# Optimization experiments

Measured on AMD Instinct MI355X. Metric: run time of the kernel, lower is better.

## Reference

```python
import jax, jax.numpy as jnp
import numpy as np

B, S, D = 4, 2048, 1024


def setup_inputs() -> dict:
    key = jax.random.key(0)
    ks = jax.random.split(key, 7)
    scale = 1.0 / np.sqrt(D)  # mimic torch Linear default init scale
    x = jax.random.normal(ks[0], (B, S, D), dtype=jnp.float32)
    Wq = jax.random.uniform(ks[1], (D, D), jnp.float32, -scale, scale)
    bq = jax.random.uniform(ks[2], (D,), jnp.float32, -scale, scale)
    Wk = jax.random.uniform(ks[3], (D, D), jnp.float32, -scale, scale)
    bk = jax.random.uniform(ks[4], (D,), jnp.float32, -scale, scale)
    Wv = jax.random.uniform(ks[5], (D, D), jnp.float32, -scale, scale)
    bv = jax.random.uniform(ks[6], (D,), jnp.float32, -scale, scale)
    return {"x": x, "Wq": Wq, "bq": bq, "Wk": Wk, "bk": bk, "Wv": Wv, "bv": bv}


def reference(x, Wq, bq, Wk, bk, Wv, bv):
    # Linear projections (torch Linear: x @ W.T + b; here W stored as [in, out])
    q = jnp.einsum("bsd,de->bse", x, Wq) + bq
    k = jnp.einsum("bsd,de->bse", x, Wk) + bk
    v = jnp.einsum("bsd,de->bse", x, Wv) + bv
    # NOTE: original module applies NO 1/sqrt(d) scaling — faithful to source.
    scores = jnp.einsum("bqd,bkd->bqk", q, k)  # [B, S, S]
    attn = jax.nn.softmax(scores, axis=-1)
    return jnp.einsum("bqk,bkd->bqd", attn, v)
```

## Files before the change

### kernel.cpp

```cpp
#include <hip/hip_runtime.h>
#include <stdint.h>

typedef unsigned short ushort_t;
typedef _Float16 f16;
typedef __attribute__((ext_vector_type(8))) _Float16 half8;
typedef __attribute__((ext_vector_type(4))) _Float16 half4;
typedef __attribute__((ext_vector_type(4))) float float4v;

#define AS1 __attribute__((address_space(1)))
#define AS3 __attribute__((address_space(3)))

static __device__ __forceinline__ void gload16(const void* g, void* l) {
    __builtin_amdgcn_global_load_lds((const AS1 unsigned int*)g,
                                     (AS3 unsigned int*)l, 16, 0, 0);
}

static __device__ __forceinline__ void barrier_nodrain() {
    __builtin_amdgcn_sched_barrier(0);
    __builtin_amdgcn_s_barrier();
    __builtin_amdgcn_sched_barrier(0);
}

template<int IM, int OUT, bool BIAS>
__global__ __launch_bounds__(256, IM == 8 ? 2 : 3)
void gemm_k(const f16* __restrict__ A, const f16* __restrict__ B,
            const float* __restrict__ bias,
            float* __restrict__ Cf, f16* __restrict__ Ch, f16* __restrict__ Vt,
            int K, int lda, int ldb, int ldc,
            long zsA, long zsB, long zsC)
{
    constexpr int R    = IM * 32;
    constexpr int AH   = R * 32;
    constexpr int NLD  = R / 64 + 2;
    extern __shared__ f16 smem[];

    const long zb = blockIdx.z;
    A += zb * zsA; B += zb * zsB;

    const int t  = threadIdx.x;
    const int bm = blockIdx.x * R;
    const int bn = blockIdx.y * 128;

    const int  srow = t >> 2;
    const int  skg  = (((t & 3) ^ ((srow >> 1) & 3)) * 8);
    const f16* gA = A + (long)(bm + srow) * lda + skg;
    const f16* gB = B + (long)(bn + srow) * ldb + skg;
    const long rstepA = (long)64 * lda;
    const long rstepB = (long)64 * ldb;

    const int lane = t & 63;
    const int wv   = t >> 6;
    const int wm   = (wv & 1) * (IM * 16);
    const int wn   = (wv >> 1) * 64;
    const int lm   = lane & 15;
    const int q    = lane >> 4;
    const int qs   = (q ^ ((lm >> 1) & 3)) * 8;

    float4v acc[IM][4];
    #pragma unroll
    for (int i = 0; i < IM; ++i)
        #pragma unroll
        for (int j = 0; j < 4; ++j)
            #pragma unroll
            for (int r = 0; r < 4; ++r) acc[i][j][r] = 0.f;

    auto stage = [&](int s) {
        const int kk  = s << 5;
        const int buf = s % 3;
        f16* dA = smem + buf * AH;
        f16* dB = smem + 3 * AH + buf * 4096;
        #pragma unroll
        for (int r = 0; r < R / 64; ++r)
            gload16(gA + kk + r * rstepA, dA + r * 2048 + t * 8);
        #pragma unroll
        for (int r = 0; r < 2; ++r)
            gload16(gB + kk + r * rstepB, dB + r * 2048 + t * 8);
    };

    const int nstage = K >> 5;
    stage(0);
    stage(1);
    for (int s = 0; s < nstage; ++s) {
        if (s + 1 < nstage) {
            __builtin_amdgcn_s_waitcnt(0x0F70 | NLD);
        } else {
            __builtin_amdgcn_s_waitcnt(0x0F70);
        }
        barrier_nodrain();

        if (s + 2 < nstage) {
            stage(s + 2);
            __builtin_amdgcn_sched_barrier(0);
        }

        const int buf = s % 3;
        const f16* sA = smem + buf * AH;
        const f16* sB = smem + 3 * AH + buf * 4096;
        half8 a[IM], b[4];
        #pragma unroll
        for (int i = 0; i < IM; ++i)
            a[i] = *(const half8*)(sA + (wm + i * 16 + lm) * 32 + qs);
        #pragma unroll
        for (int j = 0; j < 4; ++j)
            b[j] = *(const half8*)(sB + (wn + j * 16 + lm) * 32 + qs);
        #pragma unroll
        for (int i = 0; i < IM; ++i)
            #pragma unroll
            for (int j = 0; j < 4; ++j)
                acc[i][j] = __builtin_amdgcn_mfma_f32_16x16x32_f16(a[i], b[j], acc[i][j], 0, 0, 0);
    }

    #pragma unroll
    for (int i = 0; i < IM; ++i) {
        const int rowb = bm + wm + i * 16 + q * 4;
        #pragma unroll
        for (int j = 0; j < 4; ++j) {
            const int col = bn + wn + j * 16 + lm;
            const float bv_ = BIAS ? bias[col] : 0.f;
            if (OUT == 4 && col >= 2048) {
                half4 pk;
                #pragma unroll
                for (int r = 0; r < 4; ++r) pk[r] = (f16)(acc[i][j][r] + bv_);
                *(half4*)(Vt + ((long)(rowb >> 11) * 1024 + (col - 2048)) * 2048 + (rowb & 2047)) = pk;
            } else {
                #pragma unroll
                for (int r = 0; r < 4; ++r) {
                    const float val = acc[i][j][r] + bv_;
                    const int row = rowb + r;
                    if (OUT == 0)      Cf[zb * zsC + (long)row * ldc + col] = val;
                    else if (OUT == 1) Ch[zb * zsC + (long)row * ldc + col] = (f16)val;
                    else               Ch[(long)row * ldc + col] = (f16)val;
                }
            }
        }
    }
}

__global__ __launch_bounds__(256)
void preproc_k(const float* __restrict__ x,
               const float* __restrict__ Wq, const float* __restrict__ Wk,
               const float* __restrict__ Wv,
               const float* __restrict__ bq, const float* __restrict__ bk,
               const float* __restrict__ bv,
               f16* __restrict__ xh, f16* __restrict__ WT, float* __restrict__ bqkv)
{
    __shared__ float tile[64][65];
    const int bx = blockIdx.x;
    const int t  = threadIdx.x;

    if (bx < 8192) {
        const long i = ((long)bx * 256 + t) * 4;
        const float4v v = *(const float4v*)(x + i);
        half4 h;
        #pragma unroll
        for (int j = 0; j < 4; ++j) h[j] = (f16)v[j];
        *(half4*)(xh + i) = h;
    } else if (bx < 8960) {
        const int f = bx - 8192;
        const int z = f >> 8;
        const int rem = f & 255;
        const int n0 = (rem & 15) * 64;
        const int k0 = (rem >> 4) * 64;
        const float* W = (z == 0) ? Wq : (z == 1) ? Wk : Wv;
        f16* T = WT + (long)z * 1048576;
        #pragma unroll
        for (int i = 0; i < 4; ++i) {
            const int r = (t >> 4) + i * 16;
            const int c = (t & 15) * 4;
            const float4v v = *(const float4v*)(W + (long)(k0 + r) * 1024 + n0 + c);
            tile[r][c + 0] = v[0]; tile[r][c + 1] = v[1];
            tile[r][c + 2] = v[2]; tile[r][c + 3] = v[3];
        }
        __syncthreads();
        #pragma unroll
        for (int i = 0; i < 4; ++i) {
            const int nr = (t >> 4) + i * 16;
            const int c  = (t & 15) * 4;
            half4 h;
            #pragma unroll
            for (int j = 0; j < 4; ++j) h[j] = (f16)tile[c + j][nr];
            *(half4*)(T + (long)(n0 + nr) * 1024 + k0 + c) = h;
        }
    } else {
        const int i = (bx - 8960) * 256 + t;
        bqkv[i] = (i < 1024) ? bq[i] : (i < 2048) ? bk[i - 1024] : bv[i - 2048];
    }
}

__global__ __launch_bounds__(256)
void softmax_k(f16* __restrict__ Sc)
{
    const int t = threadIdx.x;
    const long row = blockIdx.x;
    half8* p = (half8*)(Sc + row * 2048);
    const half8 hv = p[t];
    float xv[8];
    #pragma unroll
    for (int j = 0; j < 8; ++j) xv[j] = (float)hv[j];

    float m = -1e30f;
    #pragma unroll
    for (int j = 0; j < 8; ++j) m = fmaxf(m, xv[j]);
    #pragma unroll
    for (int off = 32; off; off >>= 1) m = fmaxf(m, __shfl_xor(m, off, 64));
    __shared__ float r1[4], r2[4];
    if ((t & 63) == 0) r1[t >> 6] = m;
    __syncthreads();
    m = fmaxf(fmaxf(r1[0], r1[1]), fmaxf(r1[2], r1[3]));

    float s = 0.f;
    #pragma unroll
    for (int j = 0; j < 8; ++j) { xv[j] = __expf(xv[j] - m); s += xv[j]; }
    #pragma unroll
    for (int off = 32; off; off >>= 1) s += __shfl_xor(s, off, 64);
    if ((t & 63) == 0) r2[t >> 6] = s;
    __syncthreads();
    s = r2[0] + r2[1] + r2[2] + r2[3];
    const float inv = 1.f / s;

    half8 o;
    #pragma unroll
    for (int j = 0; j < 8; ++j) o[j] = (f16)(xv[j] * inv);
    p[t] = o;
}

extern "C" void kernel_launch(void* const* d_in, const int* in_sizes, int n_in,
                              void* d_out, int out_size, void* d_ws, size_t ws_size,
                              hipStream_t stream)
{
    const float* x  = (const float*)d_in[0];
    const float* Wq = (const float*)d_in[1];
    const float* bq = (const float*)d_in[2];
    const float* Wk = (const float*)d_in[3];
    const float* bk = (const float*)d_in[4];
    const float* Wv = (const float*)d_in[5];
    const float* bv = (const float*)d_in[6];
    float* out = (float*)d_out;

    char* ws = (char*)d_ws;
    const long MiB = 1024 * 1024;
    f16*   xh   = (f16*)  (ws + 0);
    f16*   WT   = (f16*)  (ws + 16 * MiB);
    float* bqkv = (float*)(ws + 22 * MiB);
    f16*   scores = (f16*) (ws + 0);
    f16*   qk     = (f16*) (ws + 64 * MiB);
    f16*   vT     = (f16*) (ws + 96 * MiB);

    preproc_k<<<8972, 256, 0, stream>>>(x, Wq, Wk, Wv, bq, bk, bv, xh, WT, bqkv);

    gemm_k<4, 4, true><<<dim3(64, 24, 1), 256, 49152, stream>>>(
        xh, WT, bqkv, nullptr, qk, vT,
        1024, 1024, 1024, 2048, 0, 0, 0);

    const long SS = (long)2048 * 2048;
    gemm_k<4, 1, false><<<dim3(16, 16, 4), 256, 49152, stream>>>(
        qk, qk + 1024, nullptr, nullptr, scores, nullptr,
        1024, 2048, 2048, 2048, SS, SS, SS);
    softmax_k<<<8192, 256, 0, stream>>>(scores);
    gemm_k<4, 0, false><<<dim3(16, 8, 4), 256, 49152, stream>>>(
        scores, vT, nullptr, out, nullptr, nullptr,
        2048, 2048, 2048, 1024, SS, (long)1024 * 2048, (long)2048 * 1024);
}
```

Before: 261.2 us.

## Add 256x256-tile 8-wave GEMM kernel with phased ping-pong pipeline for QKV and scores

Introduces a new GEMM kernel using 512 threads, 256x256 output tiles, 128KB double-buffered LDS with swizzled layout, and a phased schedule that interleaves LDS fragment loads, async global-to-LDS stages and MFMA bursts at raised priority. It replaces the 128-row tile kernel for the QKV projection and the QK^T score GEMM, aiming for higher arithmetic intensity and better overlap of memory with MFMA. Larger tiles reduce block count, so the score GEMM gets only 256 blocks, and the heavy LDS use limits occupancy, which may leave CUs underused.

```diff
diff --git a/kernel.cpp b/kernel.cpp
--- a/kernel.cpp
+++ b/kernel.cpp
@@ -19,6 +19,144 @@
     __builtin_amdgcn_sched_barrier(0);
     __builtin_amdgcn_s_barrier();
     __builtin_amdgcn_sched_barrier(0);
+}
+
+#define VMCNT(N) __builtin_amdgcn_s_waitcnt(0x0F70 | (N))
+
+#define PH_LDA(cb, ks, mlo)                                                   \
+    _Pragma("unroll")                                                         \
+    for (int m_ = 0; m_ < 4; ++m_)                                            \
+        aR[m_] = *(const half8*)(smem + (cb) + (ks)*8192 + aoff + ((mlo)+m_)*512);
+
+#define PH_LDB(cb, ks)                                                        \
+    _Pragma("unroll")                                                         \
+    for (int n_ = 0; n_ < 4; ++n_)                                            \
+        bR[n_] = *(const half8*)(smem + (cb) + (ks)*8192 + boff + n_*512);
+
+#define PH_MM(mlo)                                                            \
+    __builtin_amdgcn_s_setprio(1);                                            \
+    _Pragma("unroll")                                                         \
+    for (int m_ = 0; m_ < 4; ++m_) {                                          \
+        _Pragma("unroll")                                                     \
+        for (int n_ = 0; n_ < 4; ++n_)                                        \
+            acc[(mlo)+m_][n_] = __builtin_amdgcn_mfma_f32_16x16x32_f16(       \
+                aR[m_], bR[n_], acc[(mlo)+m_][n_], 0, 0, 0);                  \
+    }                                                                         \
+    __builtin_amdgcn_s_setprio(0);
+
+template<int OUT, bool BIAS>
+__global__ __launch_bounds__(512, 2)
+void gemm8_k(const f16* __restrict__ A, const f16* __restrict__ B,
+             const float* __restrict__ bias,
+             float* __restrict__ Cf, f16* __restrict__ Ch, f16* __restrict__ Vt,
+             int K, int lda, int ldb, int ldc,
+             long zsA, long zsB, long zsC)
+{
+    extern __shared__ f16 smem[];
+    const long zb = blockIdx.z;
+    A += zb * zsA; B += zb * zsB;
+    const int tid = threadIdx.x;
+    const int bm = blockIdx.x * 256;
+    const int bn = blockIdx.y * 256;
+
+    const int srow = tid >> 2;
+    const int sk   = (((tid & 3) ^ ((tid >> 3) & 3)) * 8);
+    const f16* gA = A + (long)(bm + srow) * lda + sk;
+    const f16* gB = B + (long)(bn + srow) * ldb + sk;
+    const long hA = (long)128 * lda;
+    const long hB = (long)128 * ldb;
+
+    const int lane = tid & 63;
+    const int wv = tid >> 6;
+    const int wm = wv >> 2;
+    const int wn = wv & 3;
+    const int lm = lane & 15;
+    const int q  = lane >> 4;
+    const int qs8  = (q ^ ((lm >> 1) & 3)) * 8;
+    const int aoff = (wm * 128 + lm) * 32 + qs8;
+    const int boff = 16384 + (wn * 64 + lm) * 32 + qs8;
+
+    float4v acc[8][4];
+    #pragma unroll
+    for (int i = 0; i < 8; ++i)
+        #pragma unroll
+        for (int j = 0; j < 4; ++j)
+            #pragma unroll
+            for (int r = 0; r < 4; ++r) acc[i][j][r] = 0.f;
+
+    auto stA = [&](int tt, int ks) {
+        f16* d = smem + (tt & 1) * 32768 + ks * 8192 + tid * 8;
+        const f16* g = gA + (long)tt * 64 + ks * 32;
+        gload16(g,      d);
+        gload16(g + hA, d + 4096);
+    };
+    auto stB = [&](int tt, int ks) {
+        f16* d = smem + (tt & 1) * 32768 + 16384 + ks * 8192 + tid * 8;
+        const f16* g = gB + (long)tt * 64 + ks * 32;
+        gload16(g,      d);
+        gload16(g + hB, d + 4096);
+    };
+
+    half8 aR[4], bR[4];
+    const int T = K >> 6;
+
+    stA(0, 0); stB(0, 0); stA(0, 1); stB(0, 1);
+    if (T > 1) { stA(1, 0); stB(1, 0); VMCNT(8); }
+    else       { VMCNT(4); }
+    barrier_nodrain();
+
+    for (int t = 0; t < T; ++t) {
+        const int cb = (t & 1) * 32768;
+        PH_LDA(cb, 0, 0)
+        PH_LDB(cb, 0)
+        if (t + 1 < T) stA(t + 1, 1);
+        barrier_nodrain();
+        PH_MM(0)
+        barrier_nodrain();
+        PH_LDA(cb, 0, 4)
+        if (t + 1 < T) { stB(t + 1, 1); VMCNT(8); }
+        else           { VMCNT(0); }
+        barrier_nodrain();
+        PH_MM(4)
+        barrier_nodrain();
+        PH_LDA(cb, 1, 0)
+        PH_LDB(cb, 1)
+        if (t + 2 < T) stA(t + 2, 0);
+        barrier_nodrain();
+        PH_MM(0)
+        barrier_nodrain();
+        PH_LDA(cb, 1, 4)
+        if (t + 2 < T) { stB(t + 2, 0); VMCNT(8); }
+        else if (t + 1 < T) { VMCNT(4); }
+        barrier_nodrain();
+        PH_MM(4)
+        barrier_nodrain();
+    }
+
+    #pragma unroll
+    for (int mf = 0; mf < 8; ++mf) {
+        const int rowb = bm + wm * 128 + mf * 16 + q * 4;
+        #pragma unroll
+        for (int nf = 0; nf < 4; ++nf) {
+            const int col = bn + wn * 64 + nf * 16 + lm;
+            const float bv_ = BIAS ? bias[col] : 0.f;
+            if (OUT == 4 && col >= 2048) {
+                half4 pk;
+                #pragma unroll
+                for (int r = 0; r < 4; ++r) pk[r] = (f16)(acc[mf][nf][r] + bv_);
+                *(half4*)(Vt + ((long)(rowb >> 11) * 1024 + (col - 2048)) * 2048 + (rowb & 2047)) = pk;
+            } else {
+                #pragma unroll
+                for (int r = 0; r < 4; ++r) {
+                    const float val = acc[mf][nf][r] + bv_;
+                    const int row = rowb + r;
+                    if (OUT == 0)      Cf[zb * zsC + (long)row * ldc + col] = val;
+                    else if (OUT == 1) Ch[zb * zsC + (long)row * ldc + col] = (f16)val;
+                    else               Ch[(long)row * ldc + col] = (f16)val;
+                }
+            }
+        }
+    }
 }
 
 template<int IM, int OUT, bool BIAS>
@@ -82,9 +220,9 @@
     stage(1);
     for (int s = 0; s < nstage; ++s) {
         if (s + 1 < nstage) {
-            __builtin_amdgcn_s_waitcnt(0x0F70 | NLD);
+            VMCNT(NLD);
         } else {
-            __builtin_amdgcn_s_waitcnt(0x0F70);
+            VMCNT(0);
         }
         barrier_nodrain();
 
@@ -248,12 +386,12 @@
 
     preproc_k<<<8972, 256, 0, stream>>>(x, Wq, Wk, Wv, bq, bk, bv, xh, WT, bqkv);
 
-    gemm_k<4, 4, true><<<dim3(64, 24, 1), 256, 49152, stream>>>(
+    gemm8_k<4, true><<<dim3(32, 12, 1), 512, 131072, stream>>>(
         xh, WT, bqkv, nullptr, qk, vT,
         1024, 1024, 1024, 2048, 0, 0, 0);
 
     const long SS = (long)2048 * 2048;
-    gemm_k<4, 1, false><<<dim3(16, 16, 4), 256, 49152, stream>>>(
+    gemm8_k<1, false><<<dim3(8, 8, 4), 512, 131072, stream>>>(
         qk, qk + 1024, nullptr, nullptr, scores, nullptr,
         1024, 2048, 2048, 2048, SS, SS, SS);
     softmax_k<<<8192, 256, 0, stream>>>(scores);
```

Measured after the change: 265.5 us. No clear change (+1.7%).
